# Kernel tuning notes

Measured on AMD Instinct MI355X. Metric: run time of the kernel, lower is better.

The kernel has to match this reference:

```python
import jax, jax.numpy as jnp
import numpy as np

TAU = 2.0        # spikingjelly LIFNode default tau
VTH = 1.0        # v_threshold
ALPHA = 2.0      # ATan surrogate alpha
NUM_HEADS = 8
N_WIN = 8
TOPK = 4


@jax.custom_vjp
def atan_heaviside(x):
    # spike = H(v - v_th), with ATan surrogate gradient
    return (x >= 0.0).astype(x.dtype)

def _ah_fwd(x):
    return atan_heaviside(x), x

def _ah_bwd(x, g):
    half_pi_alpha = np.float32(np.pi / 2.0 * ALPHA)
    return (g * (ALPHA / 2.0) / (1.0 + (half_pi_alpha * x) ** 2),)

atan_heaviside.defvjp(_ah_fwd, _ah_bwd)


def lif(x):
    """Multi-step LIF over leading time dim. decay_input=True, v_reset=0, detach_reset."""
    def step(v, xt):
        v = v + (xt - v) / TAU                      # charge
        s = atan_heaviside(v - VTH)                 # fire
        v = v * (1.0 - jax.lax.stop_gradient(s))    # hard reset (detached)
        return v, s
    _, spikes = jax.lax.scan(step, jnp.zeros_like(x[0]), x)
    return spikes


def setup_inputs() -> dict:
    key = jax.random.key(0)
    k1, k2, k3, k4, k5 = jax.random.split(key, 5)
    T, B, L, C = 4, 4, 1024, 256
    x = jax.random.normal(k1, (T, B, L, C), dtype=jnp.float32)
    w_qkv = jax.random.normal(k2, (C, 3 * C), dtype=jnp.float32) * (C ** -0.5)
    b_qkv = jax.random.normal(k3, (3 * C,), dtype=jnp.float32) * 0.02
    w_proj = jax.random.normal(k4, (C, C), dtype=jnp.float32) * (C ** -0.5)
    b_proj = jax.random.normal(k5, (C,), dtype=jnp.float32) * 0.02
    return {"x": x, "w_qkv": w_qkv, "b_qkv": b_qkv, "w_proj": w_proj, "b_proj": b_proj}


def reference(x, w_qkv, b_qkv, w_proj, b_proj):
    T, B, L, C = x.shape
    hd = C // NUM_HEADS
    win = L // N_WIN
    scale = hd ** -0.5

    # --- region-level routing (on raw input summed over time) ---
    xs = x.sum(axis=0).reshape(B, N_WIN, win, C)
    region = xs.sum(axis=2)                                  # [B, n_win, C]
    attn_r = jnp.einsum('bnc,bmc->bnm', region, region) * (C ** -0.5)
    _, idx = jax.lax.top_k(attn_r, TOPK)                     # [B, n_win, topk] int32

    # --- qkv + LIF spiking ---
    qkv = x @ w_qkv + b_qkv                                  # [T,B,L,3C]
    q, k, v = jnp.split(qkv, 3, axis=-1)
    q, k, v = lif(q), lif(k), lif(v)
    q = q.reshape(T, B, N_WIN, win, NUM_HEADS, hd)
    k = k.reshape(T, B, N_WIN, win, NUM_HEADS, hd)
    v = v.reshape(T, B, N_WIN, win, NUM_HEADS, hd)

    # --- gather routed KV windows (vectorized; topk-major concat like torch.cat) ---
    b_idx = jnp.arange(B)[:, None, None]                     # [B,1,1]
    k_g = k[:, b_idx, idx].reshape(T, B, N_WIN, TOPK * win, NUM_HEADS, hd)
    v_g = v[:, b_idx, idx].reshape(T, B, N_WIN, TOPK * win, NUM_HEADS, hd)

    # --- windowed attention over gathered keys ---
    attn = jnp.einsum('tbnqhd,tbnkhd->tbnhqk', q, k_g) * scale
    attn = jax.nn.softmax(attn, axis=-1)
    out = jnp.einsum('tbnhqk,tbnkhd->tbnqhd', attn, v_g).reshape(T, B, L, C)

    out = lif(out @ w_proj + b_proj)
    return out
```

## Files before the change

### kernel.cpp

```cpp
#include <hip/hip_runtime.h>
#include <cstdint>
#include <cstddef>

#define TT 4
#define BB 4
#define LL 1024
#define CC 256
#define HH 8
#define HD 32
#define NWIN 8
#define WIN 128
#define TOPKN 4
#define C3 768

__global__ __launch_bounds__(256) void region_kernel(const float* __restrict__ x,
                                                     float* __restrict__ region) {
    int bn = blockIdx.x;
    int b = bn >> 3, n = bn & 7;
    int c = threadIdx.x;
    float tot = 0.0f;
    for (int r = 0; r < WIN; ++r) {
        int l = n * WIN + r;
        float s = 0.0f;
        for (int t = 0; t < TT; ++t) {
            s += x[(((size_t)t * BB + b) * LL + l) * CC + c];
        }
        tot += s;
    }
    region[(size_t)bn * CC + c] = tot;
}

__global__ __launch_bounds__(64) void route_kernel(const float* __restrict__ region,
                                                   int* __restrict__ idx) {
    int b = blockIdx.x;
    __shared__ float reg[NWIN][CC];
    __shared__ float attn_r[NWIN][NWIN];
    int tid = threadIdx.x;
    for (int e = tid; e < NWIN * CC; e += 64)
        reg[e >> 8][e & 255] = region[(size_t)b * NWIN * CC + e];
    __syncthreads();
    int n = tid >> 3, m = tid & 7;
    float s = 0.0f;
    for (int c = 0; c < CC; ++c) s += reg[n][c] * reg[m][c];
    attn_r[n][m] = s * 0.0625f;
    __syncthreads();
    if (tid < NWIN) {
        float vals[NWIN];
        for (int m2 = 0; m2 < NWIN; ++m2) vals[m2] = attn_r[tid][m2];
        for (int kk = 0; kk < TOPKN; ++kk) {
            int bi = 0; float bv = vals[0];
            for (int m2 = 1; m2 < NWIN; ++m2) {
                if (vals[m2] > bv) { bv = vals[m2]; bi = m2; }
            }
            idx[(b * NWIN + tid) * TOPKN + kk] = bi;
            vals[bi] = -INFINITY;
        }
    }
}

__global__ __launch_bounds__(256, 2) void gemm_bias(const float* __restrict__ A,
                                                    const float* __restrict__ W,
                                                    const float* __restrict__ bias,
                                                    float* __restrict__ C,
                                                    int M, int N, int K) {
    const int BM = 128, BN = 128, BK = 16, TM = 8, TN = 8;
    __shared__ float As[BK][BM + 4];
    __shared__ float Bs[BK][BN];
    int tid = threadIdx.x;
    int tx = tid & 15, ty = tid >> 4;
    int bm = blockIdx.x * BM, bn = blockIdx.y * BN;
    float acc[TM][TN] = {};
    for (int k0 = 0; k0 < K; k0 += BK) {
#pragma unroll
        for (int it = 0; it < 2; ++it) {
            int i = it * 256 + tid;
            int row = i >> 2, kc = (i & 3) * 4;
            float4 v = *(const float4*)(A + (size_t)(bm + row) * K + k0 + kc);
            As[kc + 0][row] = v.x; As[kc + 1][row] = v.y;
            As[kc + 2][row] = v.z; As[kc + 3][row] = v.w;
        }
#pragma unroll
        for (int it = 0; it < 2; ++it) {
            int i = it * 256 + tid;
            int kr = i >> 5, nc = (i & 31) * 4;
            float4 v = *(const float4*)(W + (size_t)(k0 + kr) * N + bn + nc);
            *(float4*)&Bs[kr][nc] = v;
        }
        __syncthreads();
#pragma unroll
        for (int kk = 0; kk < BK; ++kk) {
            float a[TM], bb[TN];
            const float4* ap = (const float4*)&As[kk][ty * TM];
            float4 a0 = ap[0], a1 = ap[1];
            a[0]=a0.x; a[1]=a0.y; a[2]=a0.z; a[3]=a0.w;
            a[4]=a1.x; a[5]=a1.y; a[6]=a1.z; a[7]=a1.w;
            const float4* bp = (const float4*)&Bs[kk][tx * TN];
            float4 b0 = bp[0], b1 = bp[1];
            bb[0]=b0.x; bb[1]=b0.y; bb[2]=b0.z; bb[3]=b0.w;
            bb[4]=b1.x; bb[5]=b1.y; bb[6]=b1.z; bb[7]=b1.w;
#pragma unroll
            for (int i = 0; i < TM; ++i)
#pragma unroll
                for (int j = 0; j < TN; ++j)
                    acc[i][j] = fmaf(a[i], bb[j], acc[i][j]);
        }
        __syncthreads();
    }
#pragma unroll
    for (int i = 0; i < TM; ++i) {
        int row = bm + ty * TM + i;
        int col = bn + tx * TN;
        float4 o0 = make_float4(acc[i][0] + bias[col + 0], acc[i][1] + bias[col + 1],
                                acc[i][2] + bias[col + 2], acc[i][3] + bias[col + 3]);
        float4 o1 = make_float4(acc[i][4] + bias[col + 4], acc[i][5] + bias[col + 5],
                                acc[i][6] + bias[col + 6], acc[i][7] + bias[col + 7]);
        *(float4*)&C[(size_t)row * N + col]     = o0;
        *(float4*)&C[(size_t)row * N + col + 4] = o1;
    }
}

__global__ __launch_bounds__(256) void lif_kernel(const float* src, float* dst, size_t stride) {
    size_t i = ((size_t)blockIdx.x * blockDim.x + threadIdx.x) * 4;
    float v[4] = {0.f, 0.f, 0.f, 0.f};
    for (int t = 0; t < TT; ++t) {
        float4 xv4 = *(const float4*)(src + (size_t)t * stride + i);
        float xv[4] = {xv4.x, xv4.y, xv4.z, xv4.w};
        float sp[4];
#pragma unroll
        for (int j = 0; j < 4; ++j) {
            v[j] = v[j] + (xv[j] - v[j]) * 0.5f;
            bool fire = (v[j] >= 1.0f);
            sp[j] = fire ? 1.0f : 0.0f;
            v[j] = fire ? 0.0f : v[j];
        }
        *(float4*)(dst + (size_t)t * stride + i) = make_float4(sp[0], sp[1], sp[2], sp[3]);
    }
}

__global__ __launch_bounds__(256) void pack_kernel(const float* __restrict__ spk,
                                                   uint32_t* __restrict__ pk) {
    size_t g = (size_t)blockIdx.x * 256 + threadIdx.x;
    int row = (int)(g >> 9);
    int col = (int)(g & 511);
    float v = spk[(size_t)row * C3 + col];
    unsigned long long m = __ballot(v >= 0.5f);
    int lane = threadIdx.x & 63;
    if ((lane & 31) == 0)
        pk[(size_t)row * 16 + (col >> 5)] = (lane < 32) ? (uint32_t)m : (uint32_t)(m >> 32);
}

__global__ __launch_bounds__(256) void attn_sm(const uint32_t* __restrict__ pk,
                                               const int* __restrict__ idxws,
                                               float2* __restrict__ amz) {
    int bid = blockIdx.x;
    int hp = bid & 3, n = (bid >> 2) & 7, b = (bid >> 5) & 3, t = bid >> 7;
    __shared__ uint32_t kbs[2][512];
    int tid = threadIdx.x;
    int q = tid & 127, h = tid >> 7;
    int lbase = (t * BB + b) * LL;

    const int* ip = idxws + (b * NWIN + n) * TOPKN;
    int s0r = ip[0], s1r = ip[1], s2r = ip[2], s3r = ip[3];

#pragma unroll 4
    for (int e = tid; e < 1024; e += 256) {
        int hh = e >> 9, kk = e & 511;
        int w = kk >> 7;
        int sw = (w == 0) ? s0r : (w == 1) ? s1r : (w == 2) ? s2r : s3r;
        int row = sw * WIN + (kk & 127);
        kbs[hh][kk] = pk[(size_t)(lbase + row) * 16 + 8 + hp * 2 + hh];
    }
    uint32_t qw = pk[(size_t)(lbase + n * WIN + q) * 16 + hp * 2 + h];
    __syncthreads();

    const float ALPHA_SC = 0.17677669529663687f;
    const uint4* kb4 = (const uint4*)kbs[h];
    int smax = 0;
#pragma unroll 8
    for (int k4 = 0; k4 < 128; ++k4) {
        uint4 w4 = kb4[k4];
        smax = max(smax, __popc(qw & w4.x));
        smax = max(smax, __popc(qw & w4.y));
        smax = max(smax, __popc(qw & w4.z));
        smax = max(smax, __popc(qw & w4.w));
    }
    float am = __fmul_rn((float)smax, ALPHA_SC);
    float Z = 0.0f;
#pragma unroll 4
    for (int k4 = 0; k4 < 128; ++k4) {
        uint4 w4 = kb4[k4];
        Z += expf(__fsub_rn(__fmul_rn((float)__popc(qw & w4.x), ALPHA_SC), am));
        Z += expf(__fsub_rn(__fmul_rn((float)__popc(qw & w4.y), ALPHA_SC), am));
        Z += expf(__fsub_rn(__fmul_rn((float)__popc(qw & w4.z), ALPHA_SC), am));
        Z += expf(__fsub_rn(__fmul_rn((float)__popc(qw & w4.w), ALPHA_SC), am));
    }
    amz[(size_t)(lbase + n * WIN + q) * HH + hp * 2 + h] = make_float2(am, Z);
}

__global__ __launch_bounds__(128, 2) void attn_pv(const float* __restrict__ spk,
                                                  const uint32_t* __restrict__ pk,
                                                  const int* __restrict__ idxws,
                                                  const float2* __restrict__ amz,
                                                  float* __restrict__ out) {
    int bid = blockIdx.x;
    int h = bid & 1, hp = (bid >> 1) & 3, n = (bid >> 3) & 7, b = (bid >> 6) & 3, t = bid >> 8;
    __shared__ float    Vlds[WIN][32];
    __shared__ float    ptab[33][WIN];
    __shared__ uint32_t kbs[4 * WIN];
    int tid = threadIdx.x;
    int qg = tid & 63, dh = tid >> 6;
    int lbase = (t * BB + b) * LL;

    const int* ip = idxws + (b * NWIN + n) * TOPKN;
    int s0r = ip[0], s1r = ip[1], s2r = ip[2], s3r = ip[3];

#pragma unroll 4
    for (int e = tid; e < 512; e += 128) {
        int w = e >> 7;
        int sw = (w == 0) ? s0r : (w == 1) ? s1r : (w == 2) ? s2r : s3r;
        int row = sw * WIN + (e & 127);
        kbs[e] = pk[(size_t)(lbase + row) * 16 + 8 + hp * 2 + h];
    }
    uint32_t qw0 = pk[(size_t)(lbase + n * WIN + qg) * 16 + hp * 2 + h];
    uint32_t qw1 = pk[(size_t)(lbase + n * WIN + qg + 64) * 16 + hp * 2 + h];

    {
        float2 az = amz[(size_t)(lbase + n * WIN + tid) * HH + hp * 2 + h];
        const float ALPHA_SC = 0.17677669529663687f;
        for (int s = 0; s <= 32; ++s)
            ptab[s][tid] = expf(__fsub_rn(__fmul_rn((float)s, ALPHA_SC), az.x)) / az.y;
    }

    const float* vsrc = spk + (size_t)lbase * C3 + 512 + hp * 64 + h * 32
                        + (size_t)(tid >> 3) * C3 + (tid & 7) * 4;
    float* vdst = &Vlds[tid >> 3][(tid & 7) * 4];

    float4 st[8];
    {
        const float* src = vsrc + (size_t)s0r * (WIN * C3);
#pragma unroll
        for (int it = 0; it < 8; ++it)
            st[it] = *(const float4*)(src + (size_t)it * 16 * C3);
#pragma unroll
        for (int it = 0; it < 8; ++it)
            *(float4*)(vdst + it * 16 * 32) = st[it];
    }
    __syncthreads();

    float acc0[16], acc1[16];
#pragma unroll
    for (int d = 0; d < 16; ++d) { acc0[d] = 0.0f; acc1[d] = 0.0f; }

    const uint4* kb4 = (const uint4*)kbs;
    const float* vb = &Vlds[0][dh * 16];

#pragma unroll
    for (int w = 0; w < 4; ++w) {
        if (w < 3) {
            int swn = (w == 0) ? s1r : (w == 1) ? s2r : s3r;
            const float* src = vsrc + (size_t)swn * (WIN * C3);
#pragma unroll
            for (int it = 0; it < 8; ++it)
                st[it] = *(const float4*)(src + (size_t)it * 16 * C3);
        }

        const uint4* kw4 = kb4 + w * 32;
        const float* pr = vb;
#pragma unroll 2
        for (int g = 0; g < 32; ++g) {
            uint4 kw = kw4[g];
#pragma unroll
            for (int j = 0; j < 4; ++j) {
                uint32_t kwj = (j == 0) ? kw.x : (j == 1) ? kw.y : (j == 2) ? kw.z : kw.w;
                float P0 = ptab[__popc(qw0 & kwj)][qg];
                float P1 = ptab[__popc(qw1 & kwj)][qg + 64];
                const float4* vp = (const float4*)(pr + j * 32);
                float4 v0 = vp[0], v1 = vp[1], v2 = vp[2], v3 = vp[3];
                acc0[ 0] = fmaf(P0, v0.x, acc0[ 0]);  acc1[ 0] = fmaf(P1, v0.x, acc1[ 0]);
                acc0[ 1] = fmaf(P0, v0.y, acc0[ 1]);  acc1[ 1] = fmaf(P1, v0.y, acc1[ 1]);
                acc0[ 2] = fmaf(P0, v0.z, acc0[ 2]);  acc1[ 2] = fmaf(P1, v0.z, acc1[ 2]);
                acc0[ 3] = fmaf(P0, v0.w, acc0[ 3]);  acc1[ 3] = fmaf(P1, v0.w, acc1[ 3]);
                acc0[ 4] = fmaf(P0, v1.x, acc0[ 4]);  acc1[ 4] = fmaf(P1, v1.x, acc1[ 4]);
                acc0[ 5] = fmaf(P0, v1.y, acc0[ 5]);  acc1[ 5] = fmaf(P1, v1.y, acc1[ 5]);
                acc0[ 6] = fmaf(P0, v1.z, acc0[ 6]);  acc1[ 6] = fmaf(P1, v1.z, acc1[ 6]);
                acc0[ 7] = fmaf(P0, v1.w, acc0[ 7]);  acc1[ 7] = fmaf(P1, v1.w, acc1[ 7]);
                acc0[ 8] = fmaf(P0, v2.x, acc0[ 8]);  acc1[ 8] = fmaf(P1, v2.x, acc1[ 8]);
                acc0[ 9] = fmaf(P0, v2.y, acc0[ 9]);  acc1[ 9] = fmaf(P1, v2.y, acc1[ 9]);
                acc0[10] = fmaf(P0, v2.z, acc0[10]);  acc1[10] = fmaf(P1, v2.z, acc1[10]);
                acc0[11] = fmaf(P0, v2.w, acc0[11]);  acc1[11] = fmaf(P1, v2.w, acc1[11]);
                acc0[12] = fmaf(P0, v3.x, acc0[12]);  acc1[12] = fmaf(P1, v3.x, acc1[12]);
                acc0[13] = fmaf(P0, v3.y, acc0[13]);  acc1[13] = fmaf(P1, v3.y, acc1[13]);
                acc0[14] = fmaf(P0, v3.z, acc0[14]);  acc1[14] = fmaf(P1, v3.z, acc1[14]);
                acc0[15] = fmaf(P0, v3.w, acc0[15]);  acc1[15] = fmaf(P1, v3.w, acc1[15]);
            }
            pr += 128;
        }

        if (w < 3) {
            __syncthreads();
#pragma unroll
            for (int it = 0; it < 8; ++it)
                *(float4*)(vdst + it * 16 * 32) = st[it];
            __syncthreads();
        }
    }

    size_t ob0 = (size_t)(lbase + n * WIN + qg) * CC + (hp * 2 + h) * 32 + dh * 16;
    size_t ob1 = ob0 + (size_t)64 * CC;
#pragma unroll
    for (int d = 0; d < 16; ++d) out[ob0 + d] = acc0[d];
#pragma unroll
    for (int d = 0; d < 16; ++d) out[ob1 + d] = acc1[d];
}

extern "C" void kernel_launch(void* const* d_in, const int* in_sizes, int n_in,
                              void* d_out, int out_size, void* d_ws, size_t ws_size,
                              hipStream_t stream) {
    const float* x      = (const float*)d_in[0];
    const float* w_qkv  = (const float*)d_in[1];
    const float* b_qkv  = (const float*)d_in[2];
    const float* w_proj = (const float*)d_in[3];
    const float* b_proj = (const float*)d_in[4];
    float* ws = (float*)d_ws;

    float* qkv      = ws;
    float* attn_out = ws + 12582912;
    float* proj     = ws + 16777216;
    uint32_t* pkb   = (uint32_t*)proj;
    float* region   = ws + 20971520;
    int*   idxp     = (int*)(ws + 20979712);
    float2* amzp    = (float2*)(ws + 20979840);
    float* outp     = (float*)d_out;

    region_kernel<<<dim3(BB * NWIN), dim3(256), 0, stream>>>(x, region);
    route_kernel<<<dim3(BB), dim3(64), 0, stream>>>(region, idxp);
    gemm_bias<<<dim3(128, 6), dim3(256), 0, stream>>>(x, w_qkv, b_qkv, qkv,
                                                      TT * BB * LL, C3, CC);
    lif_kernel<<<dim3(3072), dim3(256), 0, stream>>>(qkv, qkv, (size_t)BB * LL * C3);
    pack_kernel<<<dim3(32768), dim3(256), 0, stream>>>(qkv, pkb);
    attn_sm<<<dim3(TT * BB * NWIN * 4), dim3(256), 0, stream>>>(pkb, idxp, amzp);
    attn_pv<<<dim3(TT * BB * NWIN * 4 * 2), dim3(128), 0, stream>>>(qkv, pkb, idxp, amzp, attn_out);
    gemm_bias<<<dim3(128, 2), dim3(256), 0, stream>>>(attn_out, w_proj, b_proj, proj,
                                                      TT * BB * LL, CC, CC);
    lif_kernel<<<dim3(1024), dim3(256), 0, stream>>>(proj, outp, (size_t)BB * LL * CC);
}
```

Measured before the change: 289.0 us.

## Stream V windows into double-buffered LDS via direct global-to-LDS loads

In attn_pv, the V staging no longer goes through registers followed by LDS stores. It now uses global_load_lds to write 16 bytes per lane straight into shared memory. The four key windows are split into eight 64-row halves, ping-ponged between two LDS buffers, so the next half loads while the current one is consumed. This frees the 8 float4 staging registers and removes the explicit LDS store pass, at the cost of more barrier and vmcnt-wait points per block.

```diff
diff --git a/kernel.cpp b/kernel.cpp
--- a/kernel.cpp
+++ b/kernel.cpp
@@ -204,7 +204,7 @@
                                                   float* __restrict__ out) {
     int bid = blockIdx.x;
     int h = bid & 1, hp = (bid >> 1) & 3, n = (bid >> 3) & 7, b = (bid >> 6) & 3, t = bid >> 8;
-    __shared__ float    Vlds[WIN][32];
+    __shared__ __align__(16) float Vlds[2][64][32];
     __shared__ float    ptab[33][WIN];
     __shared__ uint32_t kbs[4 * WIN];
     int tid = threadIdx.x;
@@ -212,12 +212,13 @@
     int lbase = (t * BB + b) * LL;
 
     const int* ip = idxws + (b * NWIN + n) * TOPKN;
-    int s0r = ip[0], s1r = ip[1], s2r = ip[2], s3r = ip[3];
+    int sidx[TOPKN];
+    sidx[0] = ip[0]; sidx[1] = ip[1]; sidx[2] = ip[2]; sidx[3] = ip[3];
 
 #pragma unroll 4
     for (int e = tid; e < 512; e += 128) {
         int w = e >> 7;
-        int sw = (w == 0) ? s0r : (w == 1) ? s1r : (w == 2) ? s2r : s3r;
+        int sw = sidx[w];
         int row = sw * WIN + (e & 127);
         kbs[e] = pk[(size_t)(lbase + row) * 16 + 8 + hp * 2 + h];
     }
@@ -233,41 +234,42 @@
 
     const float* vsrc = spk + (size_t)lbase * C3 + 512 + hp * 64 + h * 32
                         + (size_t)(tid >> 3) * C3 + (tid & 7) * 4;
-    float* vdst = &Vlds[tid >> 3][(tid & 7) * 4];
-
-    float4 st[8];
-    {
-        const float* src = vsrc + (size_t)s0r * (WIN * C3);
-#pragma unroll
-        for (int it = 0; it < 8; ++it)
-            st[it] = *(const float4*)(src + (size_t)it * 16 * C3);
-#pragma unroll
-        for (int it = 0; it < 8; ++it)
-            *(float4*)(vdst + it * 16 * 32) = st[it];
-    }
+    int wvoff = (tid >> 6) * 1024;
+
+#define STAGE_HALF(hw_)                                                              \
+    do {                                                                             \
+        int hw = (hw_);                                                              \
+        const float* src = vsrc + (size_t)sidx[hw >> 1] * (WIN * C3)                 \
+                                + (size_t)(hw & 1) * 64 * C3;                        \
+        char* lbasep = (char*)(&Vlds[hw & 1][0][0]) + wvoff;                         \
+        _Pragma("unroll")                                                            \
+        for (int it = 0; it < 4; ++it) {                                             \
+            __builtin_amdgcn_global_load_lds(                                        \
+                (const __attribute__((address_space(1))) void*)(src + (size_t)it * 16 * C3), \
+                (__attribute__((address_space(3))) void*)(lbasep + it * 2048),       \
+                16, 0, 0);                                                           \
+        }                                                                            \
+    } while (0)
+
+    STAGE_HALF(0);
+
+    float acc0[16], acc1[16];
+#pragma unroll
+    for (int d = 0; d < 16; ++d) { acc0[d] = 0.0f; acc1[d] = 0.0f; }
+
+    asm volatile("s_waitcnt vmcnt(0)" ::: "memory");
     __syncthreads();
 
-    float acc0[16], acc1[16];
-#pragma unroll
-    for (int d = 0; d < 16; ++d) { acc0[d] = 0.0f; acc1[d] = 0.0f; }
-
     const uint4* kb4 = (const uint4*)kbs;
-    const float* vb = &Vlds[0][dh * 16];
-
-#pragma unroll
-    for (int w = 0; w < 4; ++w) {
-        if (w < 3) {
-            int swn = (w == 0) ? s1r : (w == 1) ? s2r : s3r;
-            const float* src = vsrc + (size_t)swn * (WIN * C3);
-#pragma unroll
-            for (int it = 0; it < 8; ++it)
-                st[it] = *(const float4*)(src + (size_t)it * 16 * C3);
-        }
-
-        const uint4* kw4 = kb4 + w * 32;
-        const float* pr = vb;
-#pragma unroll 2
-        for (int g = 0; g < 32; ++g) {
+
+#pragma unroll
+    for (int hw = 0; hw < 8; ++hw) {
+        if (hw < 7) STAGE_HALF(hw + 1);
+
+        const uint4* kw4 = kb4 + hw * 16;
+        const float* pr = &Vlds[hw & 1][0][dh * 16];
+#pragma unroll 4
+        for (int g = 0; g < 16; ++g) {
             uint4 kw = kw4[g];
 #pragma unroll
             for (int j = 0; j < 4; ++j) {
@@ -296,14 +298,10 @@
             pr += 128;
         }
 
-        if (w < 3) {
-            __syncthreads();
-#pragma unroll
-            for (int it = 0; it < 8; ++it)
-                *(float4*)(vdst + it * 16 * 32) = st[it];
-            __syncthreads();
-        }
-    }
+        asm volatile("s_waitcnt vmcnt(0)" ::: "memory");
+        __syncthreads();
+    }
+#undef STAGE_HALF
 
     size_t ob0 = (size_t)(lbase + n * WIN + qg) * CC + (hp * 2 + h) * 32 + dh * 16;
     size_t ob1 = ob0 + (size_t)64 * CC;
```

New measurement: 286.5 us. Within noise of the previous version (-0.9%).
